# Kernel tuning notes

Measured on AMD Instinct MI355X. Metric: run time of the kernel, lower is better.

## Reference

```python
import jax, jax.numpy as jnp
import numpy as np

N, E, DIN, DH, DOUT, NG = 50000, 800000, 128, 128, 64, 128
EPS = 1e-5
SLOPE = 0.2  # PyG GATConv default negative_slope


def _gat(x, src, dst, W, a_s, a_d, b, heads, out_c, concat):
    n = x.shape[0]
    xp = (x @ W).reshape(n, heads, out_c)            # [N,H,C]
    e_src = (xp * a_s[None]).sum(-1)                  # [N,H]
    e_dst = (xp * a_d[None]).sum(-1)                  # [N,H]
    al = e_src[src] + e_dst[dst]                      # [E,H]
    al = jnp.where(al > 0, al, SLOPE * al)            # leaky_relu
    amax = jax.ops.segment_max(al, dst, num_segments=n)
    w = jnp.exp(al - amax[dst])                       # segment softmax (stable)
    den = jax.ops.segment_sum(w, dst, num_segments=n)
    msg = w[:, :, None] * xp[src]                     # [E,H,C]
    out = jax.ops.segment_sum(msg, dst, num_segments=n) / den[:, :, None]
    out = out.reshape(n, heads * out_c) if concat else out.mean(axis=1)
    return out + b


def _bn(h, g, be):
    m = h.mean(axis=0)
    v = h.var(axis=0)  # biased var, as in torch BN training mode
    return (h - m) / jnp.sqrt(v + EPS) * g + be


def setup_inputs() -> dict:
    key = jax.random.key(0)
    ks = jax.random.split(key, 12)
    x = jax.random.normal(ks[0], (N, DIN), dtype=jnp.float32)
    edge_index = jax.random.randint(ks[1], (2, E), 0, N, dtype=jnp.int64)
    graph_pool = jax.random.uniform(ks[2], (NG, N), dtype=jnp.float32) * (2.0 / N)
    s = 0.1
    return {
        "x": x, "edge_index": edge_index, "graph_pool": graph_pool,
        "W1": jax.random.normal(ks[3], (DIN, DH), dtype=jnp.float32) * s,
        "as1": jax.random.normal(ks[4], (1, DH), dtype=jnp.float32) * s,
        "ad1": jax.random.normal(ks[5], (1, DH), dtype=jnp.float32) * s,
        "b1": jnp.zeros((DH,), jnp.float32),
        "g1": jnp.ones((DH,), jnp.float32), "be1": jnp.zeros((DH,), jnp.float32),
        "W2": jax.random.normal(ks[6], (DH, DH), dtype=jnp.float32) * s,
        "as2": jax.random.normal(ks[7], (1, DH), dtype=jnp.float32) * s,
        "ad2": jax.random.normal(ks[8], (1, DH), dtype=jnp.float32) * s,
        "b2": jnp.zeros((DH,), jnp.float32),
        "g2": jnp.ones((DH,), jnp.float32), "be2": jnp.zeros((DH,), jnp.float32),
        "W3": jax.random.normal(ks[9], (DH, DOUT), dtype=jnp.float32) * s,
        "as3": jax.random.normal(ks[10], (1, DOUT), dtype=jnp.float32) * s,
        "ad3": jax.random.normal(ks[11], (1, DOUT), dtype=jnp.float32) * s,
        "b3": jnp.zeros((DOUT,), jnp.float32),
    }


def reference(x, edge_index, graph_pool,
              W1, as1, ad1, b1, g1, be1,
              W2, as2, ad2, b2, g2, be2,
              W3, as3, ad3, b3):
    n = x.shape[0]
    loops = jnp.arange(n, dtype=edge_index.dtype)  # PyG add_self_loops=True
    src = jnp.concatenate([edge_index[0], loops])
    dst = jnp.concatenate([edge_index[1], loops])
    h = _gat(x, src, dst, W1, as1, ad1, b1, 1, DH, True)
    h = jax.nn.relu(_bn(h, g1, be1))
    h = _gat(h, src, dst, W2, as2, ad2, b2, 1, DH, True)
    h = jax.nn.relu(_bn(h, g2, be2))
    h_nodes = _gat(h, src, dst, W3, as3, ad3, b3, 1, DOUT, False)
    h_pooled = graph_pool @ h_nodes  # sparse.mm == matmul mathematically
    return (h_pooled, h_nodes)
```

## Files before the change

kernel.cpp:

```cpp
#include <hip/hip_runtime.h>
#include <hip/hip_bf16.h>

#define DIN 128
#define DH  128
#define DOUT 64
#define NGR 128
#define EPSV 1e-5f
#define SLOPE 0.2f
#define BSH 7
#define NBMAX 512
#define BCAP 3584
#define POOLB 128

typedef __attribute__((ext_vector_type(8))) short short8;
typedef __attribute__((ext_vector_type(4))) float float4v;

__device__ __forceinline__ unsigned short f2bf(float f) {
    union { float f; unsigned int u; } v; v.f = f;
    unsigned int r = (v.u + 0x7FFFu + ((v.u >> 16) & 1u)) >> 16;
    return (unsigned short)r;
}
__device__ __forceinline__ unsigned short f2bf_f(float f) {
    return (unsigned short)((__float_as_uint(f) + 0x8000u) >> 16);
}
__device__ __forceinline__ float bf_lo(unsigned int u) { return __uint_as_float(u << 16); }
__device__ __forceinline__ float bf_hi(unsigned int u) { return __uint_as_float(u & 0xFFFF0000u); }

__device__ __forceinline__ void pack_one(const float* W, unsigned short* PW, int cout, int t) {
    int lane = t & 63;
    int ks   = (t >> 6) & 3;
    int nt   = t >> 8;
    int nn   = nt * 16 + (lane & 15);
    int k0   = ks * 32 + (lane >> 4) * 8;
    unsigned int pk[4];
#pragma unroll
    for (int p = 0; p < 4; ++p) {
        unsigned short lo = f2bf(W[(k0 + 2 * p) * cout + nn]);
        unsigned short hi = f2bf(W[(k0 + 2 * p + 1) * cout + nn]);
        pk[p] = ((unsigned int)hi << 16) | lo;
    }
    *(uint4*)&PW[(size_t)t * 8] = make_uint4(pk[0], pk[1], pk[2], pk[3]);
}

__global__ __launch_bounds__(256) void front_a_kernel(
    const int* __restrict__ ei, int* __restrict__ bucket_cnt, int2* __restrict__ binned,
    int E, int T, int nb, int binBlocks,
    const float* __restrict__ W1, unsigned short* __restrict__ PW1,
    const float* __restrict__ W2, unsigned short* __restrict__ PW2,
    const float* __restrict__ W3, unsigned short* __restrict__ PW3)
{
    if ((int)blockIdx.x >= binBlocks) {
        int t = ((int)blockIdx.x - binBlocks) * 256 + (int)threadIdx.x;
        if (t < 2048)      pack_one(W1, PW1, 128, t);
        else if (t < 4096) pack_one(W2, PW2, 128, t - 2048);
        else if (t < 5120) pack_one(W3, PW3, 64,  t - 4096);
        return;
    }
    __shared__ int hist[NBMAX], base[NBMAX], cur[NBMAX];
    for (int i = threadIdx.x; i < nb; i += 256) hist[i] = 0;
    __syncthreads();
    int start = blockIdx.x * 8192;
    int endc  = start + 8192; if (endc > T) endc = T;
    for (int e = start + threadIdx.x; e < endc; e += 256) {
        int d = (e < E) ? ei[E + e] : (e - E);
        atomicAdd(&hist[d >> BSH], 1);
    }
    __syncthreads();
    for (int i = threadIdx.x; i < nb; i += 256) {
        int h = hist[i];
        cur[i] = 0;
        if (h) base[i] = atomicAdd(&bucket_cnt[i], h);
    }
    __syncthreads();
    for (int e = start + threadIdx.x; e < endc; e += 256) {
        int s, d;
        if (e < E) { s = ei[e]; d = ei[E + e]; }
        else       { s = e - E; d = s; }
        int b = d >> BSH;
        int off = atomicAdd(&cur[b], 1);
        binned[(size_t)b * BCAP + base[b] + off] = make_int2(s, d);
    }
}

template <int COUT, int BNIN>
__device__ __forceinline__ void gemm_es_body(
    unsigned short* Xs, float* sSc, float* sSh, int row0,
    const void* __restrict__ Xv, const unsigned short* __restrict__ PW,
    const float* __restrict__ a_s, const float* __restrict__ a_d,
    const float* __restrict__ bnsum, const float* __restrict__ g,
    const float* __restrict__ be, float invn,
    unsigned short* __restrict__ XPB, float* __restrict__ e_src, float* __restrict__ e_dst, int n)
{
    constexpr int NT = COUT / 16;
    int tid = threadIdx.x;

    if constexpr (BNIN) {
        if (tid < 128) {
            float mean = bnsum[tid] * invn;
            float var  = bnsum[128 + tid] * invn - mean * mean;
            float sc   = g[tid] * rsqrtf(var + EPSV);
            sSc[tid] = sc;
            sSh[tid] = be[tid] - mean * sc;
        }
        __syncthreads();
        const unsigned short* H = (const unsigned short*)Xv;
        for (int i = tid; i < 64 * 16; i += 256) {
            int r  = i >> 4;
            int c8 = (i & 15) * 8;
            uint4 u = make_uint4(0, 0, 0, 0);
            if (row0 + r < n) u = *(const uint4*)&H[(size_t)(row0 + r) * 128 + c8];
            unsigned int uu[4] = {u.x, u.y, u.z, u.w};
            unsigned int out[4];
#pragma unroll
            for (int p = 0; p < 4; ++p) {
                int c = c8 + 2 * p;
                float a  = fmaxf(bf_lo(uu[p]) * sSc[c] + sSh[c], 0.f);
                float bq = fmaxf(bf_hi(uu[p]) * sSc[c + 1] + sSh[c + 1], 0.f);
                out[p] = ((unsigned int)f2bf_f(bq) << 16) | f2bf_f(a);
            }
            *(uint4*)&Xs[r * 136 + c8] = make_uint4(out[0], out[1], out[2], out[3]);
        }
    } else {
        const float* X = (const float*)Xv;
        for (int i = tid; i < 64 * 32; i += 256) {
            int r  = i >> 5;
            int k4 = (i & 31) * 4;
            float4 v = make_float4(0.f, 0.f, 0.f, 0.f);
            if (row0 + r < n) v = *(const float4*)&X[(size_t)(row0 + r) * 128 + k4];
            uint2 pk;
            pk.x = ((unsigned int)f2bf_f(v.y) << 16) | f2bf_f(v.x);
            pk.y = ((unsigned int)f2bf_f(v.w) << 16) | f2bf_f(v.z);
            *(uint2*)&Xs[r * 136 + k4] = pk;
        }
    }
    __syncthreads();

    int wv   = tid >> 6;
    int lane = tid & 63;
    int m0   = wv * 16;
    int cl   = lane & 15;
    int q    = lane >> 4;

    float4v acc[NT] = {};
#pragma unroll
    for (int ks = 0; ks < 4; ++ks) {
        short8 af = *(const short8*)&Xs[(m0 + cl) * 136 + ks * 32 + q * 8];
#pragma unroll
        for (int nt = 0; nt < NT; ++nt) {
            short8 bf = *(const short8*)&PW[(size_t)((nt * 4 + ks) * 64 + lane) * 8];
            acc[nt] = __builtin_amdgcn_mfma_f32_16x16x32_bf16(af, bf, acc[nt], 0, 0, 0);
        }
    }

    float asv[NT], adv[NT];
#pragma unroll
    for (int nt = 0; nt < NT; ++nt) {
        asv[nt] = a_s[nt * 16 + cl];
        adv[nt] = a_d[nt * 16 + cl];
    }
#pragma unroll
    for (int reg = 0; reg < 4; ++reg) {
        int m = row0 + m0 + q * 4 + reg;
        if (m >= n) continue;
        float ps = 0.f, pd = 0.f;
        size_t base = (size_t)m * COUT;
#pragma unroll
        for (int nt = 0; nt < NT; ++nt) {
            float v = acc[nt][reg];
            XPB[base + nt * 16 + cl] = f2bf_f(v);
            ps += v * asv[nt];
            pd += v * adv[nt];
        }
        ps += __shfl_xor(ps, 1); pd += __shfl_xor(pd, 1);
        ps += __shfl_xor(ps, 2); pd += __shfl_xor(pd, 2);
        ps += __shfl_xor(ps, 4); pd += __shfl_xor(pd, 4);
        ps += __shfl_xor(ps, 8); pd += __shfl_xor(pd, 8);
        if (cl == 0) {
            e_src[m] = ps;
            e_dst[m] = pd;
        }
    }
}

template <int COUT, int BNIN>
__global__ __launch_bounds__(256) void gemm_es_kernel(
    const void* __restrict__ Xv, const unsigned short* __restrict__ PW,
    const float* __restrict__ a_s, const float* __restrict__ a_d,
    const float* __restrict__ bnsum, const float* __restrict__ g,
    const float* __restrict__ be, float invn,
    unsigned short* __restrict__ XPB, float* __restrict__ e_src, float* __restrict__ e_dst, int n)
{
    __shared__ unsigned short Xs[64 * 136];
    __shared__ float sSc[128], sSh[128];
    gemm_es_body<COUT, BNIN>(Xs, sSc, sSh, blockIdx.x * 64,
                             Xv, PW, a_s, a_d, bnsum, g, be, invn, XPB, e_src, e_dst, n);
}

__global__ __launch_bounds__(256) void front_b_kernel(
    const int2* __restrict__ binned, const int* __restrict__ bucket_cnt,
    int* __restrict__ row_ptr, int* __restrict__ col_src, int n, int T, int nbcsr,
    const float* __restrict__ X, const unsigned short* __restrict__ PW,
    const float* __restrict__ a_s, const float* __restrict__ a_d,
    unsigned short* __restrict__ XPB, float* __restrict__ e_src, float* __restrict__ e_dst)
{
    __shared__ __align__(16) char smraw[64 * 136 * 2];
    int tid = threadIdx.x;

    if ((int)blockIdx.x < nbcsr) {
        int* cnt = (int*)smraw;
        int* rnk = cnt + 128;
        int* rp  = rnk + 128;
        int* sc  = rp + 128;
        int* red = sc + 128;
        int b = blockIdx.x;
        int node0 = b << BSH;
        const int2* bin = &binned[(size_t)b * BCAP];
        int nb_edges = bucket_cnt[b];

        int part = 0;
        for (int i = tid; i < b; i += 256) part += bucket_cnt[i];
        red[tid] = part;
        if (tid < 128) cnt[tid] = 0;
        __syncthreads();
#pragma unroll
        for (int s2 = 128; s2 > 0; s2 >>= 1) {
            if (tid < s2) red[tid] += red[tid + s2];
            __syncthreads();
        }
        int lo = red[0];

        for (int i = tid; i < nb_edges; i += 256)
            atomicAdd(&cnt[bin[i].y - node0], 1);
        __syncthreads();
        if (tid < 128) sc[tid] = cnt[tid];
        __syncthreads();
        for (int d2 = 1; d2 < 128; d2 <<= 1) {
            int t = 0;
            if (tid < 128 && tid >= d2) t = sc[tid - d2];
            __syncthreads();
            if (tid < 128) sc[tid] += t;
            __syncthreads();
        }
        if (tid < 128) {
            int excl = sc[tid] - cnt[tid];
            int r = lo + excl;
            rp[tid] = r;
            rnk[tid] = 0;
            int node = node0 + tid;
            if (node < n) row_ptr[node] = r;
        }
        if (b == 0 && tid == 0) row_ptr[n] = T;
        __syncthreads();
        for (int i = tid; i < nb_edges; i += 256) {
            int2 e = bin[i];
            int local = e.y - node0;
            int r = atomicAdd(&rnk[local], 1);
            col_src[rp[local] + r] = e.x;
        }
    } else {
        unsigned short* Xs = (unsigned short*)smraw;
        gemm_es_body<128, 0>(Xs, nullptr, nullptr, ((int)blockIdx.x - nbcsr) * 64,
                             X, PW, a_s, a_d, nullptr, nullptr, nullptr, 0.f,
                             XPB, e_src, e_dst, n);
    }
}

template <int COUT, int OUTBF>
__global__ __launch_bounds__(256) void gat_aggregate_kernel(
    const unsigned short* __restrict__ XPB, const float* __restrict__ e_src,
    const float* __restrict__ e_dst, const int* __restrict__ row_ptr,
    const int* __restrict__ col_src, const float* __restrict__ bias,
    void* __restrict__ OUT, int n)
{
    __shared__ int2 sw[4][64];
    int wave = threadIdx.x >> 6;
    int lane = threadIdx.x & 63;
    int d = blockIdx.x * 4 + wave;
    if (d >= n) return;
    int start = row_ptr[d];
    int end   = row_ptr[d + 1];
    float ed  = e_dst[d];

    float denl = 0.f;
    float2 acc2 = make_float2(0.f, 0.f);
    float acc1 = 0.f;
    const unsigned int* xpu = (const unsigned int*)XPB;

    for (int base = start; base < end; base += 64) {
        int t = base + lane;
        int s_l = 0; float w_l = 0.f;
        if (t < end) {
            s_l = col_src[t];
            float a = e_src[s_l] + ed;
            a = (a > 0.f) ? a : SLOPE * a;
            w_l = __expf(a);
        }
        denl += w_l;
        sw[wave][lane] = make_int2(s_l, __float_as_int(w_l));
        int cnt = end - base; if (cnt > 64) cnt = 64;

        int j = 0;
        for (; j + 7 < cnt; j += 8) {
            int ss[8]; float wwv[8];
#pragma unroll
            for (int p = 0; p < 8; ++p) {
                int2 e = sw[wave][j + p];
                ss[p]  = e.x;
                wwv[p] = __int_as_float(e.y);
            }
            if (COUT == 128) {
                unsigned int us[8];
#pragma unroll
                for (int p = 0; p < 8; ++p) us[p] = xpu[(size_t)ss[p] * 64 + lane];
#pragma unroll
                for (int p = 0; p < 8; ++p) {
                    acc2.x += wwv[p] * bf_lo(us[p]);
                    acc2.y += wwv[p] * bf_hi(us[p]);
                }
            } else {
                float xs[8];
#pragma unroll
                for (int p = 0; p < 8; ++p)
                    xs[p] = __uint_as_float((unsigned int)XPB[(size_t)ss[p] * COUT + lane] << 16);
#pragma unroll
                for (int p = 0; p < 8; ++p) acc1 += wwv[p] * xs[p];
            }
        }
        for (; j + 3 < cnt; j += 4) {
            int ss[4]; float wwv[4];
#pragma unroll
            for (int p = 0; p < 4; ++p) {
                int2 e = sw[wave][j + p];
                ss[p]  = e.x;
                wwv[p] = __int_as_float(e.y);
            }
            if (COUT == 128) {
                unsigned int us[4];
#pragma unroll
                for (int p = 0; p < 4; ++p) us[p] = xpu[(size_t)ss[p] * 64 + lane];
#pragma unroll
                for (int p = 0; p < 4; ++p) {
                    acc2.x += wwv[p] * bf_lo(us[p]);
                    acc2.y += wwv[p] * bf_hi(us[p]);
                }
            } else {
#pragma unroll
                for (int p = 0; p < 4; ++p) {
                    float xv = __uint_as_float((unsigned int)XPB[(size_t)ss[p] * COUT + lane] << 16);
                    acc1 += wwv[p] * xv;
                }
            }
        }
        for (; j < cnt; ++j) {
            int2 e = sw[wave][j];
            int   s = e.x;
            float w = __int_as_float(e.y);
            if (COUT == 128) {
                unsigned int u = xpu[(size_t)s * 64 + lane];
                acc2.x += w * bf_lo(u);
                acc2.y += w * bf_hi(u);
            } else {
                acc1 += w * __uint_as_float((unsigned int)XPB[(size_t)s * COUT + lane] << 16);
            }
        }
    }

#pragma unroll
    for (int off = 1; off < 64; off <<= 1) denl += __shfl_xor(denl, off);
    float inv = 1.f / denl;

    if (COUT == 128) {
        float ox = acc2.x * inv + bias[2 * lane + 0];
        float oy = acc2.y * inv + bias[2 * lane + 1];
        if (OUTBF) {
            unsigned int o = ((unsigned int)f2bf_f(oy) << 16) | f2bf_f(ox);
            ((unsigned int*)OUT)[(size_t)d * 64 + lane] = o;
        } else {
            ((float2*)OUT)[(size_t)d * 64 + lane] = make_float2(ox, oy);
        }
    } else {
        ((float*)OUT)[(size_t)d * COUT + lane] = acc1 * inv + bias[lane];
    }
}

__global__ __launch_bounds__(256) void bn_stats_bf_kernel(const unsigned short* __restrict__ H,
                                                          float* __restrict__ sums, int n) {
    __shared__ float sh[1024];
    int c2  = threadIdx.x & 63;
    int grp = threadIdx.x >> 6;
    float sx = 0.f, sy = 0.f, qx = 0.f, qy = 0.f;
    const unsigned int* Hu = (const unsigned int*)H;
    for (int i = blockIdx.x * 4 + grp; i < n; i += gridDim.x * 4) {
        unsigned int u = Hu[(size_t)i * 64 + c2];
        float a = bf_lo(u), b = bf_hi(u);
        sx += a; qx += a * a;
        sy += b; qy += b * b;
    }
    sh[threadIdx.x]       = sx;
    sh[256 + threadIdx.x] = sy;
    sh[512 + threadIdx.x] = qx;
    sh[768 + threadIdx.x] = qy;
    __syncthreads();
    if (grp == 0) {
#pragma unroll
        for (int g2 = 1; g2 < 4; ++g2) {
            sx += sh[g2 * 64 + c2];
            sy += sh[256 + g2 * 64 + c2];
            qx += sh[512 + g2 * 64 + c2];
            qy += sh[768 + g2 * 64 + c2];
        }
        atomicAdd(&sums[2 * c2],       sx);
        atomicAdd(&sums[2 * c2 + 1],   sy);
        atomicAdd(&sums[128 + 2 * c2],     qx);
        atomicAdd(&sums[128 + 2 * c2 + 1], qy);
    }
}

__global__ __launch_bounds__(256) void pool_partial_kernel(
    const float* __restrict__ GP, const float* __restrict__ HN,
    float* __restrict__ partial, int n)
{
    __shared__ float hn_lds[64 * 64];
    __shared__ float gp_lds[128 * 68];

    int tid = threadIdx.x;
    int cg  = tid & 15;
    int gg  = tid >> 4;
    int c0  = cg * 4;

    float acc[8][4] = {};
    int nchunk = (n + 127) >> 7;

    for (int blk = blockIdx.x; blk < nchunk; blk += gridDim.x) {
        for (int sub = 0; sub < 2; ++sub) {
            int k0 = blk * 128 + sub * 64;
            for (int i = tid; i < 64 * 16; i += 256) {
                int kk = i >> 4;
                int c4 = (i & 15) * 4;
                int gk = k0 + kk;
                float4 v = make_float4(0.f, 0.f, 0.f, 0.f);
                if (gk < n) v = *(const float4*)&HN[(size_t)gk * 64 + c4];
                *(float4*)&hn_lds[kk * 64 + c4] = v;
            }
            for (int i = tid; i < 128 * 16; i += 256) {
                int g  = i >> 4;
                int k4 = (i & 15) * 4;
                int gk = k0 + k4;
                float4 v = make_float4(0.f, 0.f, 0.f, 0.f);
                if (gk < n) v = *(const float4*)&GP[(size_t)g * n + gk];
                *(float4*)&gp_lds[g * 68 + k4] = v;
            }
            __syncthreads();

#pragma unroll 4
            for (int k = 0; k < 64; ++k) {
                float4 hv = *(const float4*)&hn_lds[k * 64 + c0];
#pragma unroll
                for (int j = 0; j < 8; ++j) {
                    float gv = gp_lds[(gg + 16 * j) * 68 + k];
                    acc[j][0] += gv * hv.x;
                    acc[j][1] += gv * hv.y;
                    acc[j][2] += gv * hv.z;
                    acc[j][3] += gv * hv.w;
                }
            }
            __syncthreads();
        }
    }

    float* po = &partial[(size_t)blockIdx.x * (NGR * DOUT)];
#pragma unroll
    for (int j = 0; j < 8; ++j) {
        *(float4*)&po[(gg + 16 * j) * 64 + c0] =
            make_float4(acc[j][0], acc[j][1], acc[j][2], acc[j][3]);
    }
}

__global__ __launch_bounds__(256) void pool_reduce_kernel(
    const float* __restrict__ partial, float* __restrict__ OUT, int nblk)
{
    int i = blockIdx.x * 256 + threadIdx.x;
    float s0 = 0.f, s1 = 0.f, s2 = 0.f, s3 = 0.f;
    int p = 0;
    for (; p + 3 < nblk; p += 4) {
        s0 += partial[(size_t)(p + 0) * (NGR * DOUT) + i];
        s1 += partial[(size_t)(p + 1) * (NGR * DOUT) + i];
        s2 += partial[(size_t)(p + 2) * (NGR * DOUT) + i];
        s3 += partial[(size_t)(p + 3) * (NGR * DOUT) + i];
    }
    for (; p < nblk; ++p) s0 += partial[(size_t)p * (NGR * DOUT) + i];
    OUT[i] = (s0 + s1) + (s2 + s3);
}

extern "C" void kernel_launch(void* const* d_in, const int* in_sizes, int n_in,
                              void* d_out, int out_size, void* d_ws, size_t ws_size,
                              hipStream_t stream) {
    const float* x   = (const float*)d_in[0];
    const int*   ei  = (const int*)d_in[1];
    const float* gp  = (const float*)d_in[2];
    const float* W1  = (const float*)d_in[3];
    const float* as1 = (const float*)d_in[4];
    const float* ad1 = (const float*)d_in[5];
    const float* b1  = (const float*)d_in[6];
    const float* g1  = (const float*)d_in[7];
    const float* be1 = (const float*)d_in[8];
    const float* W2  = (const float*)d_in[9];
    const float* as2 = (const float*)d_in[10];
    const float* ad2 = (const float*)d_in[11];
    const float* b2  = (const float*)d_in[12];
    const float* g2  = (const float*)d_in[13];
    const float* be2 = (const float*)d_in[14];
    const float* W3  = (const float*)d_in[15];
    const float* as3 = (const float*)d_in[16];
    const float* ad3 = (const float*)d_in[17];
    const float* b3  = (const float*)d_in[18];

    const int N = in_sizes[0] / DIN;
    const int E = in_sizes[1] / 2;
    const int T = E + N;
    const int NB = (N + 127) >> BSH;

    char* ws = (char*)d_ws;
    auto take = [&](size_t bytes) {
        char* p = ws;
        ws += (bytes + 511) & ~(size_t)511;
        return p;
    };
    unsigned short* xpb = (unsigned short*)take((size_t)N * 128 * 2);
    unsigned short* h   = (unsigned short*)take((size_t)N * 128 * 2);
    float* pool_s  = (float*)take((size_t)POOLB * NGR * DOUT * 4);
    float* esd     = (float*)take((size_t)2 * N * 4);
    float* e_src   = esd;
    float* e_dst   = esd + N;
    int*   row_ptr = (int*)take((size_t)(N + 1) * 4);
    int*   col_src = (int*)take((size_t)T * 4);
    int2*  binned  = (int2*)take((size_t)NB * BCAP * 8);
    int*   zero_rgn      = (int*)take((size_t)(NBMAX + 1 + 512) * 4);
    int*   bucket_cnt    = zero_rgn;
    float* bnsum1        = (float*)(zero_rgn + NBMAX + 1);
    float* bnsum2        = bnsum1 + 256;
    unsigned short* pw1 = (unsigned short*)take((size_t)128 * 128 * 2);
    unsigned short* pw2 = (unsigned short*)take((size_t)128 * 128 * 2);
    unsigned short* pw3 = (unsigned short*)take((size_t)128 * 64 * 2);

    float* outp = (float*)d_out;
    float* hn   = outp + NGR * DOUT;

    hipMemsetAsync(zero_rgn, 0, (size_t)(NBMAX + 1 + 512) * 4, stream);

    const int binBlocks = (T + 8191) / 8192;
    front_a_kernel<<<binBlocks + 20, 256, 0, stream>>>(ei, bucket_cnt, binned, E, T, NB, binBlocks,
                                                       W1, pw1, W2, pw2, W3, pw3);

    const int gx = (N + 63) / 64;
    const float invn = 1.f / N;

    front_b_kernel<<<NB + gx, 256, 0, stream>>>(binned, bucket_cnt, row_ptr, col_src, N, T, NB,
                                                x, pw1, as1, ad1, xpb, e_src, e_dst);

    gat_aggregate_kernel<128, 1><<<(N + 3) / 4, 256, 0, stream>>>(xpb, e_src, e_dst, row_ptr, col_src, b1, h, N);
    bn_stats_bf_kernel<<<240, 256, 0, stream>>>(h, bnsum1, N);

    gemm_es_kernel<128, 1><<<gx, 256, 0, stream>>>(h, pw2, as2, ad2,
        bnsum1, g1, be1, invn, xpb, e_src, e_dst, N);
    gat_aggregate_kernel<128, 1><<<(N + 3) / 4, 256, 0, stream>>>(xpb, e_src, e_dst, row_ptr, col_src, b2, h, N);
    bn_stats_bf_kernel<<<240, 256, 0, stream>>>(h, bnsum2, N);

    gemm_es_kernel<64, 1><<<gx, 256, 0, stream>>>(h, pw3, as3, ad3,
        bnsum2, g2, be2, invn, xpb, e_src, e_dst, N);
    gat_aggregate_kernel<64, 0><<<(N + 3) / 4, 256, 0, stream>>>(xpb, e_src, e_dst, row_ptr, col_src, b3, hn, N);

    const int nchunk = (N + 127) / 128;
    const int pb = nchunk < POOLB ? nchunk : POOLB;
    pool_partial_kernel<<<pb, 256, 0, stream>>>(gp, hn, pool_s, N);
    pool_reduce_kernel<<<(NGR * DOUT + 255) / 256, 256, 0, stream>>>(pool_s, outp, pb);
}
```

Measured before the change: 407.4 us.

## Replace pooling FMA kernels with a bf16 MFMA kernel using atomic accumulation

The final graph-pooling matmul moves from a scalar-FMA partial-sum kernel plus a separate reduce kernel to a single bf16 MFMA kernel. Each block handles one 128-node chunk and atomically adds its tile into a zeroed output. To feed it, the last aggregation kernel also writes a transposed bf16 copy of the node outputs. This is meant to cut the pooling compute cost, use many more blocks, and drop the reduce launch. In exchange it adds strided, uncoalesced transposed writes in the aggregation kernel, heavy atomic traffic on the 128x64 output, and bf16 rounding of graph_pool and the node features.

```diff
diff --git a/kernel.cpp b/kernel.cpp
--- a/kernel.cpp
+++ b/kernel.cpp
@@ -10,7 +10,6 @@
 #define BSH 7
 #define NBMAX 512
 #define BCAP 3584
-#define POOLB 128
 
 typedef __attribute__((ext_vector_type(8))) short short8;
 typedef __attribute__((ext_vector_type(4))) float float4v;
@@ -270,7 +269,7 @@
     const unsigned short* __restrict__ XPB, const float* __restrict__ e_src,
     const float* __restrict__ e_dst, const int* __restrict__ row_ptr,
     const int* __restrict__ col_src, const float* __restrict__ bias,
-    void* __restrict__ OUT, int n)
+    void* __restrict__ OUT, unsigned short* __restrict__ HNT, int n)
 {
     __shared__ int2 sw[4][64];
     int wave = threadIdx.x >> 6;
@@ -379,7 +378,9 @@
             ((float2*)OUT)[(size_t)d * 64 + lane] = make_float2(ox, oy);
         }
     } else {
-        ((float*)OUT)[(size_t)d * COUT + lane] = acc1 * inv + bias[lane];
+        float o = acc1 * inv + bias[lane];
+        ((float*)OUT)[(size_t)d * COUT + lane] = o;
+        HNT[(size_t)lane * n + d] = f2bf_f(o);
     }
 }
 
@@ -416,80 +417,70 @@
     }
 }
 
-__global__ __launch_bounds__(256) void pool_partial_kernel(
-    const float* __restrict__ GP, const float* __restrict__ HN,
-    float* __restrict__ partial, int n)
+__global__ __launch_bounds__(256) void pool_mfma_kernel(
+    const float* __restrict__ GP, const unsigned short* __restrict__ HNT,
+    float* __restrict__ OUTP, int n)
 {
-    __shared__ float hn_lds[64 * 64];
-    __shared__ float gp_lds[128 * 68];
-
+    __shared__ unsigned short gp_s[128 * 136];
+    __shared__ unsigned short ht_s[64 * 136];
     int tid = threadIdx.x;
-    int cg  = tid & 15;
-    int gg  = tid >> 4;
-    int c0  = cg * 4;
-
-    float acc[8][4] = {};
-    int nchunk = (n + 127) >> 7;
-
-    for (int blk = blockIdx.x; blk < nchunk; blk += gridDim.x) {
-        for (int sub = 0; sub < 2; ++sub) {
-            int k0 = blk * 128 + sub * 64;
-            for (int i = tid; i < 64 * 16; i += 256) {
-                int kk = i >> 4;
-                int c4 = (i & 15) * 4;
-                int gk = k0 + kk;
-                float4 v = make_float4(0.f, 0.f, 0.f, 0.f);
-                if (gk < n) v = *(const float4*)&HN[(size_t)gk * 64 + c4];
-                *(float4*)&hn_lds[kk * 64 + c4] = v;
-            }
-            for (int i = tid; i < 128 * 16; i += 256) {
-                int g  = i >> 4;
-                int k4 = (i & 15) * 4;
-                int gk = k0 + k4;
-                float4 v = make_float4(0.f, 0.f, 0.f, 0.f);
-                if (gk < n) v = *(const float4*)&GP[(size_t)g * n + gk];
-                *(float4*)&gp_lds[g * 68 + k4] = v;
-            }
-            __syncthreads();
-
-#pragma unroll 4
-            for (int k = 0; k < 64; ++k) {
-                float4 hv = *(const float4*)&hn_lds[k * 64 + c0];
-#pragma unroll
-                for (int j = 0; j < 8; ++j) {
-                    float gv = gp_lds[(gg + 16 * j) * 68 + k];
-                    acc[j][0] += gv * hv.x;
-                    acc[j][1] += gv * hv.y;
-                    acc[j][2] += gv * hv.z;
-                    acc[j][3] += gv * hv.w;
-                }
-            }
-            __syncthreads();
-        }
-    }
-
-    float* po = &partial[(size_t)blockIdx.x * (NGR * DOUT)];
-#pragma unroll
-    for (int j = 0; j < 8; ++j) {
-        *(float4*)&po[(gg + 16 * j) * 64 + c0] =
-            make_float4(acc[j][0], acc[j][1], acc[j][2], acc[j][3]);
-    }
-}
-
-__global__ __launch_bounds__(256) void pool_reduce_kernel(
-    const float* __restrict__ partial, float* __restrict__ OUT, int nblk)
-{
-    int i = blockIdx.x * 256 + threadIdx.x;
-    float s0 = 0.f, s1 = 0.f, s2 = 0.f, s3 = 0.f;
-    int p = 0;
-    for (; p + 3 < nblk; p += 4) {
-        s0 += partial[(size_t)(p + 0) * (NGR * DOUT) + i];
-        s1 += partial[(size_t)(p + 1) * (NGR * DOUT) + i];
-        s2 += partial[(size_t)(p + 2) * (NGR * DOUT) + i];
-        s3 += partial[(size_t)(p + 3) * (NGR * DOUT) + i];
-    }
-    for (; p < nblk; ++p) s0 += partial[(size_t)p * (NGR * DOUT) + i];
-    OUT[i] = (s0 + s1) + (s2 + s3);
+    int k0  = blockIdx.x * 128;
+
+    for (int i = tid; i < 128 * 8; i += 256) {
+        int r  = i >> 3;
+        int kk = (i & 7) * 16;
+        int gk = k0 + kk;
+        const float* src = &GP[(size_t)r * n + gk];
+        unsigned int pk[8];
+#pragma unroll
+        for (int q2 = 0; q2 < 4; ++q2) {
+            float4 v = make_float4(0.f, 0.f, 0.f, 0.f);
+            if (gk + q2 * 4 < n) v = *(const float4*)&src[q2 * 4];
+            pk[2 * q2 + 0] = ((unsigned int)f2bf_f(v.y) << 16) | f2bf_f(v.x);
+            pk[2 * q2 + 1] = ((unsigned int)f2bf_f(v.w) << 16) | f2bf_f(v.z);
+        }
+        *(uint4*)&gp_s[r * 136 + kk]     = make_uint4(pk[0], pk[1], pk[2], pk[3]);
+        *(uint4*)&gp_s[r * 136 + kk + 8] = make_uint4(pk[4], pk[5], pk[6], pk[7]);
+    }
+    for (int i = tid; i < 64 * 16; i += 256) {
+        int r  = i >> 4;
+        int kk = (i & 15) * 8;
+        int gk = k0 + kk;
+        uint4 v = make_uint4(0, 0, 0, 0);
+        if (gk < n) v = *(const uint4*)&HNT[(size_t)r * n + gk];
+        *(uint4*)&ht_s[r * 136 + kk] = v;
+    }
+    __syncthreads();
+
+    int wv = tid >> 6, lane = tid & 63, cl = lane & 15, q = lane >> 4;
+    float4v acc[4][2] = {};
+#pragma unroll
+    for (int ks = 0; ks < 4; ++ks) {
+        short8 bfr[2];
+#pragma unroll
+        for (int j = 0; j < 2; ++j)
+            bfr[j] = *(const short8*)&gp_s[((wv * 2 + j) * 16 + cl) * 136 + ks * 32 + q * 8];
+#pragma unroll
+        for (int mt = 0; mt < 4; ++mt) {
+            short8 af = *(const short8*)&ht_s[(mt * 16 + cl) * 136 + ks * 32 + q * 8];
+#pragma unroll
+            for (int j = 0; j < 2; ++j)
+                acc[mt][j] = __builtin_amdgcn_mfma_f32_16x16x32_bf16(af, bfr[j], acc[mt][j], 0, 0, 0);
+        }
+    }
+
+#pragma unroll
+    for (int mt = 0; mt < 4; ++mt) {
+#pragma unroll
+        for (int j = 0; j < 2; ++j) {
+            int g = (wv * 2 + j) * 16 + cl;
+            int c = mt * 16 + q * 4;
+            float* dst = &OUTP[g * 64 + c];
+#pragma unroll
+            for (int reg = 0; reg < 4; ++reg)
+                atomicAdd(&dst[reg], acc[mt][j][reg]);
+        }
+    }
 }
 
 extern "C" void kernel_launch(void* const* d_in, const int* in_sizes, int n_in,
@@ -528,7 +519,7 @@
     };
     unsigned short* xpb = (unsigned short*)take((size_t)N * 128 * 2);
     unsigned short* h   = (unsigned short*)take((size_t)N * 128 * 2);
-    float* pool_s  = (float*)take((size_t)POOLB * NGR * DOUT * 4);
+    unsigned short* hnt = (unsigned short*)take((size_t)64 * N * 2);
     float* esd     = (float*)take((size_t)2 * N * 4);
     float* e_src   = esd;
     float* e_dst   = esd + N;
@@ -547,6 +538,7 @@
     float* hn   = outp + NGR * DOUT;
 
     hipMemsetAsync(zero_rgn, 0, (size_t)(NBMAX + 1 + 512) * 4, stream);
+    hipMemsetAsync(outp, 0, (size_t)NGR * DOUT * 4, stream);
 
     const int binBlocks = (T + 8191) / 8192;
     front_a_kernel<<<binBlocks + 20, 256, 0, stream>>>(ei, bucket_cnt, binned, E, T, NB, binBlocks,
@@ -558,20 +550,18 @@
     front_b_kernel<<<NB + gx, 256, 0, stream>>>(binned, bucket_cnt, row_ptr, col_src, N, T, NB,
                                                 x, pw1, as1, ad1, xpb, e_src, e_dst);
 
-    gat_aggregate_kernel<128, 1><<<(N + 3) / 4, 256, 0, stream>>>(xpb, e_src, e_dst, row_ptr, col_src, b1, h, N);
+    gat_aggregate_kernel<128, 1><<<(N + 3) / 4, 256, 0, stream>>>(xpb, e_src, e_dst, row_ptr, col_src, b1, h, nullptr, N);
     bn_stats_bf_kernel<<<240, 256, 0, stream>>>(h, bnsum1, N);
 
     gemm_es_kernel<128, 1><<<gx, 256, 0, stream>>>(h, pw2, as2, ad2,
         bnsum1, g1, be1, invn, xpb, e_src, e_dst, N);
-    gat_aggregate_kernel<128, 1><<<(N + 3) / 4, 256, 0, stream>>>(xpb, e_src, e_dst, row_ptr, col_src, b2, h, N);
+    gat_aggregate_kernel<128, 1><<<(N + 3) / 4, 256, 0, stream>>>(xpb, e_src, e_dst, row_ptr, col_src, b2, h, nullptr, N);
     bn_stats_bf_kernel<<<240, 256, 0, stream>>>(h, bnsum2, N);
 
     gemm_es_kernel<64, 1><<<gx, 256, 0, stream>>>(h, pw3, as3, ad3,
         bnsum2, g2, be2, invn, xpb, e_src, e_dst, N);
-    gat_aggregate_kernel<64, 0><<<(N + 3) / 4, 256, 0, stream>>>(xpb, e_src, e_dst, row_ptr, col_src, b3, hn, N);
+    gat_aggregate_kernel<64, 0><<<(N + 3) / 4, 256, 0, stream>>>(xpb, e_src, e_dst, row_ptr, col_src, b3, hn, hnt, N);
 
     const int nchunk = (N + 127) / 128;
-    const int pb = nchunk < POOLB ? nchunk : POOLB;
-    pool_partial_kernel<<<pb, 256, 0, stream>>>(gp, hn, pool_s, N);
-    pool_reduce_kernel<<<(NGR * DOUT + 255) / 256, 256, 0, stream>>>(pool_s, outp, pb);
-}
+    pool_mfma_kernel<<<nchunk, 256, 0, stream>>>(gp, hnt, outp, N);
+}
```

New measurement: 392.8 us. 1.04x faster.
